# Performance work log

Measured on AMD Instinct MI355X. Metric: run time of the kernel, lower is better.

Reference implementation:

```python
import jax, jax.numpy as jnp
import numpy as np
from jax import lax

PAD = 40
MAX_DISP = 40
STRIDE2 = 1
CORR_MULT = 1.0


def _correlation1d(input1, input2):
    # input1, input2: [B, C, H, W]; kernel_size=1, stride1=1
    B, C, H, W = input1.shape
    D = 2 * MAX_DISP // STRIDE2 + 1  # 81 displacement channels
    # zero-pad input2 along the width dimension
    in2p = jnp.pad(input2, ((0, 0), (0, 0), (0, 0), (PAD, PAD)))
    offsets = jnp.arange(D, dtype=jnp.int32) * STRIDE2  # start col in padded map; disp = off - PAD

    def body(carry, off):
        shifted = lax.dynamic_slice(in2p, (0, 0, 0, off), (B, C, H, W))
        # mean over channels (sumelems = kernel_size^2 * C = C)
        c = jnp.sum(input1 * shifted, axis=1) / C  # [B, H, W]
        return carry, c

    _, corr = lax.scan(body, None, offsets)  # [D, B, H, W]
    out = jnp.transpose(corr, (1, 0, 2, 3)) * CORR_MULT  # [B, D, H, W]
    return out


def setup_inputs() -> dict:
    key = jax.random.key(0)
    k1, k2 = jax.random.split(key)
    input1 = jax.random.normal(k1, (8, 256, 96, 192), dtype=jnp.float32)
    input2 = jax.random.normal(k2, (8, 256, 96, 192), dtype=jnp.float32)
    return {"input1": input1, "input2": input2}


def reference(input1, input2):
    return _correlation1d(input1, input2)
```

## Files before the change

### kernel.cpp

```cpp
#include <hip/hip_runtime.h>


typedef __attribute__((ext_vector_type(8))) short short8;
typedef __attribute__((ext_vector_type(4))) float float4v;

__device__ __forceinline__ unsigned short f2bf(float f) {
  unsigned int u = __float_as_uint(f);
  return (unsigned short)((u + 0x7FFFu + ((u >> 16) & 1u)) >> 16);
}

__device__ __forceinline__ void glds4(const float* g, float* l) {
  __builtin_amdgcn_global_load_lds(
      (const __attribute__((address_space(1))) void*)g,
      (__attribute__((address_space(3))) void*)l, 4, 0, 0);
}

__global__ __launch_bounds__(256, 3) void corr1d_kernel(
    const float* __restrict__ in1, const float* __restrict__ in2,
    float* __restrict__ out) {
  constexpr int W = 192, H = 96, C = 256, D = 81;
  constexpr int HW = H * W;
  constexpr int KC = 32;
  constexpr int SR = 194;
  constexpr int ES = 196;

  __shared__ __align__(16) float smem[2 * KC * SR];
  float* As = smem;
  float* Bs = smem + KC * SR;
  float* E  = smem;

  const int bh = blockIdx.x;
  const int b = bh / H, h = bh % H;
  const int tid = threadIdx.x;
  const int lane = tid & 63;
  const int wv = tid >> 6;
  const int l15 = lane & 15, lq = lane >> 4;
  const int base = (b * C * H + h) * W;

  float4v acc[3][6];
#pragma unroll
  for (int i = 0; i < 3; ++i)
#pragma unroll
    for (int jj = 0; jj < 6; ++jj) acc[i][jj] = (float4v){0.f, 0.f, 0.f, 0.f};

  for (int m = 0; m < C / KC; ++m) {
    const int c0 = KC * m;
    __syncthreads();

#pragma unroll
    for (int r = 0; r < 8; ++r) {
      const int k = 8 * wv + r;
      const float* g1 = in1 + base + (c0 + k) * HW + lane;
      const float* g2 = in2 + base + (c0 + k) * HW + lane;
      float* lA = As + k * SR;
      float* lB = Bs + k * SR;
#pragma unroll
      for (int g = 0; g < 3; ++g) {
        glds4(g1 + 64 * g, lA + 64 * g);
        glds4(g2 + 64 * g, lB + 64 * g);
      }
    }
    __syncthreads();

    short8 af[3];
#pragma unroll
    for (int i = 0; i < 3; ++i) {
      const float* ap = As + 48 * wv + 16 * i + l15;
      unsigned short o[8];
#pragma unroll
      for (int t = 0; t < 8; ++t) o[t] = f2bf(ap[(8 * lq + t) * SR]);
      af[i] = *(const short8*)o;
    }
#pragma unroll
    for (int jt = 0; jt < 8; ++jt) {
      const int j = 16 * (3 * wv + jt) + l15;
      const bool ok = (j >= 40) && (j < 232);
      const float* bp = Bs + (ok ? (j - 40) : 0);
      unsigned short o[8];
#pragma unroll
      for (int t = 0; t < 8; ++t) {
        float v = ok ? bp[(8 * lq + t) * SR] : 0.0f;
        o[t] = f2bf(v);
      }
      short8 bfr = *(const short8*)o;
#pragma unroll
      for (int i = 0; i < 3; ++i) {
        const int jj = jt - i;
        if (jj >= 0 && jj < 6)
          acc[i][jj] = __builtin_amdgcn_mfma_f32_16x16x32_bf16(
              af[i], bfr, acc[i][jj], 0, 0, 0);
      }
    }
  }

  const float scale = 1.0f / 256.0f;
#pragma unroll
  for (int p = 0; p < 2; ++p) {
    const int dlo = p ? 41 : 0;
    const int nd  = p ? 40 : 41;
    __syncthreads();
#pragma unroll
    for (int i = 0; i < 3; ++i)
#pragma unroll
      for (int jj = 0; jj < 6; ++jj)
#pragma unroll
        for (int r = 0; r < 4; ++r) {
          const int d = 16 * jj + l15 - 4 * lq - r;
          const int w = 48 * wv + 16 * i + 4 * lq + r;
          if (d >= dlo && d < dlo + nd)
            E[(d - dlo) * ES + w] = acc[i][jj][r] * scale;
        }
    __syncthreads();
    for (int t = tid; t < nd * 48; t += 256) {
      const int dr = t / 48, g = t % 48;
      float4v val = *(const float4v*)(E + dr * ES + 4 * g);
      *(float4v*)(out + ((b * D + dlo + dr) * H + h) * W + 4 * g) = val;
    }
  }
}

extern "C" void kernel_launch(void* const* d_in, const int* in_sizes, int n_in,
                              void* d_out, int out_size, void* d_ws, size_t ws_size,
                              hipStream_t stream) {
  const float* in1 = (const float*)d_in[0];
  const float* in2 = (const float*)d_in[1];
  float* out = (float*)d_out;
  (void)in_sizes; (void)n_in; (void)out_size; (void)d_ws; (void)ws_size;
  corr1d_kernel<<<dim3(768), dim3(256), 0, stream>>>(in1, in2, out);
}
```

Baseline: 325.5 us.

## Load A operand directly to registers, widen B LDS loads, shrink shared memory

The in1 operand is now read straight from global memory into registers for the bf16 MFMA fragments instead of being staged through LDS. in2 is staged with 16-byte global_load_lds transfers using a row-padded layout meant to reduce bank conflicts. Shared memory drops to about 24KB, the epilogue is split into three 27-row passes to fit, and launch bounds are raised to 4 blocks per CU for more occupancy. The trade-off is that the direct A loads are uncoalesced 16-wide strided accesses, which adds register pressure and global load latency.

```diff
diff --git a/kernel.cpp b/kernel.cpp
--- a/kernel.cpp
+++ b/kernel.cpp
@@ -9,24 +9,24 @@
   return (unsigned short)((u + 0x7FFFu + ((u >> 16) & 1u)) >> 16);
 }
 
-__device__ __forceinline__ void glds4(const float* g, float* l) {
+__device__ __forceinline__ void glds16(const float* g, float* l) {
   __builtin_amdgcn_global_load_lds(
       (const __attribute__((address_space(1))) void*)g,
-      (__attribute__((address_space(3))) void*)l, 4, 0, 0);
+      (__attribute__((address_space(3))) void*)l, 16, 0, 0);
 }
 
-__global__ __launch_bounds__(256, 3) void corr1d_kernel(
+__device__ __forceinline__ int rbB(int k) { return 194 * k + 2 * (k & 1); }
+
+__global__ __launch_bounds__(256, 4) void corr1d_kernel(
     const float* __restrict__ in1, const float* __restrict__ in2,
     float* __restrict__ out) {
   constexpr int W = 192, H = 96, C = 256, D = 81;
   constexpr int HW = H * W;
   constexpr int KC = 32;
-  constexpr int SR = 194;
   constexpr int ES = 196;
 
-  __shared__ __align__(16) float smem[2 * KC * SR];
-  float* As = smem;
-  float* Bs = smem + KC * SR;
+  __shared__ __align__(16) float smem[6216];
+  float* Bs = smem;
   float* E  = smem;
 
   const int bh = blockIdx.x;
@@ -43,6 +43,8 @@
 #pragma unroll
     for (int jj = 0; jj < 6; ++jj) acc[i][jj] = (float4v){0.f, 0.f, 0.f, 0.f};
 
+  const float* a_col = in1 + base + 48 * wv + l15;
+
   for (int m = 0; m < C / KC; ++m) {
     const int c0 = KC * m;
     __syncthreads();
@@ -50,36 +52,36 @@
 #pragma unroll
     for (int r = 0; r < 8; ++r) {
       const int k = 8 * wv + r;
-      const float* g1 = in1 + base + (c0 + k) * HW + lane;
-      const float* g2 = in2 + base + (c0 + k) * HW + lane;
-      float* lA = As + k * SR;
-      float* lB = Bs + k * SR;
+      if (lane < 48)
+        glds16(in2 + base + (c0 + k) * HW + 4 * lane, Bs + rbB(k));
+    }
+
+    float a_raw[3][8];
 #pragma unroll
-      for (int g = 0; g < 3; ++g) {
-        glds4(g1 + 64 * g, lA + 64 * g);
-        glds4(g2 + 64 * g, lB + 64 * g);
-      }
-    }
-    __syncthreads();
-
+    for (int i = 0; i < 3; ++i)
+#pragma unroll
+      for (int t = 0; t < 8; ++t)
+        a_raw[i][t] = a_col[(c0 + 8 * lq + t) * HW + 16 * i];
     short8 af[3];
 #pragma unroll
     for (int i = 0; i < 3; ++i) {
-      const float* ap = As + 48 * wv + 16 * i + l15;
       unsigned short o[8];
 #pragma unroll
-      for (int t = 0; t < 8; ++t) o[t] = f2bf(ap[(8 * lq + t) * SR]);
+      for (int t = 0; t < 8; ++t) o[t] = f2bf(a_raw[i][t]);
       af[i] = *(const short8*)o;
     }
+
+    __syncthreads();
+
 #pragma unroll
     for (int jt = 0; jt < 8; ++jt) {
       const int j = 16 * (3 * wv + jt) + l15;
       const bool ok = (j >= 40) && (j < 232);
-      const float* bp = Bs + (ok ? (j - 40) : 0);
+      const int col = ok ? (j - 40) : 0;
       unsigned short o[8];
 #pragma unroll
       for (int t = 0; t < 8; ++t) {
-        float v = ok ? bp[(8 * lq + t) * SR] : 0.0f;
+        float v = ok ? Bs[rbB(8 * lq + t) + col] : 0.0f;
         o[t] = f2bf(v);
       }
       short8 bfr = *(const short8*)o;
@@ -95,9 +97,8 @@
 
   const float scale = 1.0f / 256.0f;
 #pragma unroll
-  for (int p = 0; p < 2; ++p) {
-    const int dlo = p ? 41 : 0;
-    const int nd  = p ? 40 : 41;
+  for (int p = 0; p < 3; ++p) {
+    const int dlo = 27 * p;
     __syncthreads();
 #pragma unroll
     for (int i = 0; i < 3; ++i)
@@ -107,11 +108,11 @@
         for (int r = 0; r < 4; ++r) {
           const int d = 16 * jj + l15 - 4 * lq - r;
           const int w = 48 * wv + 16 * i + 4 * lq + r;
-          if (d >= dlo && d < dlo + nd)
+          if (d >= dlo && d < dlo + 27)
             E[(d - dlo) * ES + w] = acc[i][jj][r] * scale;
         }
     __syncthreads();
-    for (int t = tid; t < nd * 48; t += 256) {
+    for (int t = tid; t < 27 * 48; t += 256) {
       const int dr = t / 48, g = t % 48;
       float4v val = *(const float4v*)(E + dr * ES + 4 * g);
       *(float4v*)(out + ((b * D + dlo + dr) * H + h) * W + 4 * g) = val;
```

Result: slower. 338.2 us (+3.9%).
